# Kernel tuning notes

Hardware: AMD Instinct MI355X
Metric: run time of the kernel (lower is better)

Reference implementation:

```python
import jax, jax.numpy as jnp
import numpy as np

B, T_Q, T_K, H = 16, 1024, 1024, 1024


def _linear_params(key, fan_in, fan_out):
    kw, kb = jax.random.split(key)
    bound = 1.0 / np.sqrt(fan_in)
    W = jax.random.uniform(kw, (fan_out, fan_in), jnp.float32, -bound, bound)
    b = jax.random.uniform(kb, (fan_out,), jnp.float32, -bound, bound)
    return W, b


def setup_inputs() -> dict:
    key = jax.random.key(0)
    ks = jax.random.split(key, 6)
    query = jax.random.normal(ks[0], (B, T_Q, H), jnp.float32)
    keys = jax.random.normal(ks[1], (B, T_K, H), jnp.float32)
    values = jax.random.normal(ks[2], (B, T_K, H), jnp.float32)
    Wq, bq = _linear_params(ks[3], H, H)
    Wk, bk = _linear_params(ks[4], H, H)
    Wo, bo = _linear_params(ks[5], H, H)
    return {"query": query, "keys": keys, "values": values,
            "Wq": Wq, "bq": bq, "Wk": Wk, "bk": bk, "Wo": Wo, "bo": bo}


def reference(query, keys, values, Wq, bq, Wk, bk, Wo, bo):
    # Linear projections (torch Linear: x @ W.T + b)
    q = jnp.einsum('bth,oh->bto', query, Wq) + bq   # (B, T_Q, H)
    k = jnp.einsum('bsh,oh->bso', keys, Wk) + bk    # (B, T_K, H)
    # Unscaled scores -> softmax over key axis (dropout is identity at eval)
    scores = jnp.einsum('bto,bso->bts', q, k)       # (B, T_Q, T_K)
    attn = jax.nn.softmax(scores, axis=-1)
    ctx = jnp.einsum('bts,bsh->bth', attn, values)  # note: raw values, value_fc unused in source
    ctx = ctx / jnp.sqrt(jnp.float32(values.shape[1]))
    out = jnp.einsum('bth,oh->bto', ctx, Wo) + bo
    return out
```

## Files before the change

kernel.cpp:

```cpp
#include <hip/hip_runtime.h>
#include <math.h>

typedef __attribute__((ext_vector_type(4))) float f32x4;
typedef __attribute__((ext_vector_type(8))) _Float16 h16x8;
typedef __attribute__((ext_vector_type(8))) short s16x8;
typedef __attribute__((ext_vector_type(4))) short s16x4;

__device__ inline unsigned short f2h(float f) {
    union { _Float16 h; unsigned short u; } v; v.h = (_Float16)f; return v.u;
}
__device__ inline float h2f(unsigned short u) {
    union { unsigned short u; _Float16 h; } v; v.u = u; return (float)v.h;
}

__device__ inline void async16(const void* g, void* l) {
    __builtin_amdgcn_global_load_lds(
        (const __attribute__((address_space(1))) unsigned int*)g,
        (__attribute__((address_space(3))) unsigned int*)l, 16, 0, 0);
}

__device__ inline void xcd_swizzle(int& bx, int& by, int& bz) {
    const long gx = gridDim.x, gy = gridDim.y;
    const long nwg = gx * gy * (long)gridDim.z;
    const long hw  = ((long)blockIdx.z * gy + blockIdx.y) * gx + blockIdx.x;
    const long qq = nwg >> 3, rr = nwg & 7;
    const long xcd = hw & 7, pos = hw >> 3;
    const long lg = (xcd < rr) ? xcd * (qq + 1) + pos
                               : rr * (qq + 1) + (xcd - rr) * qq + pos;
    bx = (int)(lg % gx);
    const long rem = lg / gx;
    by = (int)(rem % gy);
    bz = (int)(rem / gy);
}

#define BM2 128
#define BN2 256
#define BK2 32

__device__ inline h16x8 ld_frag32(const char* smem, unsigned base, int row, int q) {
    const int lr = row >> 1;
    const int slot = (((row & 1) << 2) | q) ^ (lr & 7);
    return *(const h16x8*)(smem + base + (unsigned)(lr * 128 + slot * 16));
}

template<int OM>
__global__ __launch_bounds__(512, 4)
void gemm128(const unsigned short* __restrict__ A,
             const unsigned short* __restrict__ B,
             const float* __restrict__ bias,
             void* __restrict__ C, int N, int lenK, int pitch,
             long sA, long sB, long sC, long sBias, float scale)
{
    __shared__ __align__(16) char smem[49152];

    const int tid  = threadIdx.x;
    const int wv   = tid >> 6;
    const int lane = tid & 63;
    const int wr = wv >> 2, wc = wv & 3;
    const int lrow = lane & 15;
    const int kq   = lane >> 4;

    int bx, by, bz; xcd_swizzle(bx, by, bz);
    const int n0 = bx * BN2;
    const int m0 = by * BM2;

    const unsigned short* Ag = A + (long)bz * sA;
    const unsigned short* Bg = B + (long)bz * sB;
    const int NT = lenK / BK2;

    auto srcRQ = [](int i, int& r, int& q) {
        int lr = i >> 3;
        int sl = (i & 7) ^ (lr & 7);
        r = (lr << 1) | (sl >> 2);
        q = sl & 3;
    };

    auto stage = [&](int t) {
        const unsigned db = (unsigned)((t & 1) * 24576);
        {
            int r, q; srcRQ(tid, r, q);
            async16((const char*)Ag + ((long)(m0 + r) * pitch + t * BK2 + q * 8) * 2,
                    smem + db + (unsigned)(wv << 10));
        }
#pragma unroll
        for (int l = 0; l < 2; ++l) {
            int r, q; srcRQ(l * 512 + tid, r, q);
            async16((const char*)Bg + ((long)(n0 + r) * pitch + t * BK2 + q * 8) * 2,
                    smem + db + 8192u + (unsigned)(l * 8192) + (unsigned)(wv << 10));
        }
    };

    f32x4 acc[4][4];
#pragma unroll
    for (int i = 0; i < 4; ++i)
#pragma unroll
        for (int j = 0; j < 4; ++j) acc[i][j] = (f32x4){0.f, 0.f, 0.f, 0.f};

    const unsigned Abase = (unsigned)(wr * 4096);
    const unsigned Bbase = 8192u + (unsigned)(wc * 4096);

    stage(0);
    __syncthreads();

#pragma unroll 2
    for (int t = 0; t < NT; ++t) {
        const unsigned db = (unsigned)((t & 1) * 24576);
        if (t + 1 < NT) stage(t + 1);
        h16x8 afr[4], bfr[4];
#pragma unroll
        for (int f = 0; f < 4; ++f) {
            afr[f] = ld_frag32(smem, db + Abase, f * 16 + lrow, kq);
            bfr[f] = ld_frag32(smem, db + Bbase, f * 16 + lrow, kq);
        }
#pragma unroll
        for (int mi = 0; mi < 4; ++mi)
#pragma unroll
            for (int j = 0; j < 4; ++j)
                acc[mi][j] = __builtin_amdgcn_mfma_f32_16x16x32_f16(
                    afr[mi], bfr[j], acc[mi][j], 0, 0, 0);
        __syncthreads();
    }

#pragma unroll
    for (int j = 0; j < 4; ++j) {
        const int col = n0 + wc * 64 + j * 16 + lrow;
        const float bb = bias ? bias[(long)bz * sBias + col] : 0.f;
#pragma unroll
        for (int mi = 0; mi < 4; ++mi) {
#pragma unroll
            for (int r = 0; r < 4; ++r) {
                const long row = m0 + wr * 64 + mi * 16 + (lane >> 4) * 4 + r;
                const float v = acc[mi][j][r] * scale + bb;
                const long idx = (long)bz * sC + row * (long)N + col;
                if constexpr (OM == 0) ((float*)C)[idx] = v;
                else                   ((unsigned short*)C)[idx] = f2h(v);
            }
        }
    }
}


__global__ __launch_bounds__(256)
void conv2_f16(const float* __restrict__ a, const float* __restrict__ b,
               unsigned short* __restrict__ oa, unsigned short* __restrict__ ob)
{
    const long i = ((long)blockIdx.x * 256 + threadIdx.x) * 8;
    const float* in = blockIdx.y ? b : a;
    unsigned short* out = blockIdx.y ? ob : oa;
    f32x4 v0 = __builtin_nontemporal_load((const f32x4*)(in + i));
    f32x4 v1 = __builtin_nontemporal_load((const f32x4*)(in + i + 4));
    s16x8 o = {(short)f2h(v0.x), (short)f2h(v0.y), (short)f2h(v0.z), (short)f2h(v0.w),
               (short)f2h(v1.x), (short)f2h(v1.y), (short)f2h(v1.z), (short)f2h(v1.w)};
    __builtin_nontemporal_store(o, (s16x8*)(out + i));
}

__global__ __launch_bounds__(256)
void conv_f16(const float* __restrict__ in, unsigned short* __restrict__ out, int n)
{
    int i = (blockIdx.x * 256 + threadIdx.x) * 4;
    if (i >= n) return;
    f32x4 v = *(const f32x4*)(in + i);
    s16x4 o = {(short)f2h(v.x), (short)f2h(v.y), (short)f2h(v.z), (short)f2h(v.w)};
    *(s16x4*)(out + i) = o;
}

__global__ __launch_bounds__(256)
void transpose_vals(const float* __restrict__ in, unsigned short* __restrict__ out)
{
    __shared__ float tile[32][33];
    const int h0 = blockIdx.x * 32, t0 = blockIdx.y * 32;
    for (int z = blockIdx.z; z < 16; z += gridDim.z) {
        const long base = (long)z * 1024 * 1024;
        __syncthreads();
        for (int i = threadIdx.y; i < 32; i += 8)
            tile[i][threadIdx.x] = in[base + (long)(t0 + i) * 1024 + h0 + threadIdx.x];
        __syncthreads();
        for (int i = threadIdx.y; i < 32; i += 8)
            out[base + (long)(h0 + i) * 1024 + t0 + threadIdx.x] = f2h(tile[threadIdx.x][i]);
    }
}

__global__ __launch_bounds__(256)
void transpose2_f16(const float* __restrict__ inA, const float* __restrict__ inB,
                    unsigned short* __restrict__ outA, unsigned short* __restrict__ outB)
{
    __shared__ float tile[32][33];
    const float* in = blockIdx.z ? inB : inA;
    unsigned short* out = blockIdx.z ? outB : outA;
    const int h0 = blockIdx.x * 32, t0 = blockIdx.y * 32;
    for (int i = threadIdx.y; i < 32; i += 8)
        tile[i][threadIdx.x] = in[(long)(t0 + i) * 1024 + h0 + threadIdx.x];
    __syncthreads();
    for (int i = threadIdx.y; i < 32; i += 8)
        out[(long)(h0 + i) * 1024 + t0 + threadIdx.x] = f2h(tile[threadIdx.x][i]);
}

__global__ __launch_bounds__(256)
void w2_kernel(const float* __restrict__ Wk, const float* __restrict__ bq,
               float* __restrict__ w2)
{
    __shared__ float part[4][64];
    const int tx = threadIdx.x & 63;
    const int ty = threadIdx.x >> 6;
    const int h  = blockIdx.x * 64 + tx;
    float s = 0.f;
    for (int o = ty * 256; o < ty * 256 + 256; ++o)
        s = fmaf(Wk[(long)o * 1024 + h], bq[o], s);
    part[ty][tx] = s;
    __syncthreads();
    if (ty == 0) w2[h] = part[0][tx] + part[1][tx] + part[2][tx] + part[3][tx];
}

__global__ __launch_bounds__(256)
void matvec_v(const unsigned short* __restrict__ Xk, const float* __restrict__ w2,
              float* __restrict__ v)
{
    const int wave = threadIdx.x >> 6, lane = threadIdx.x & 63;
    const long row = (long)blockIdx.x * 4 + wave;
    const unsigned short* p = Xk + row * 1024 + lane * 16;
    float s = 0.f;
#pragma unroll
    for (int c = 0; c < 2; ++c) {
        s16x8 hv = *(const s16x8*)(p + c * 8);
#pragma unroll
        for (int e = 0; e < 8; ++e)
            s = fmaf(h2f((unsigned short)hv[e]), w2[lane * 16 + c * 8 + e], s);
    }
#pragma unroll
    for (int off = 1; off < 64; off <<= 1) s += __shfl_xor(s, off);
    if (lane == 0) v[row] = s;
}

__global__ __launch_bounds__(256)
void reduce4(const float* __restrict__ p, unsigned short* __restrict__ MT)
{
    const long i = ((long)blockIdx.x * 256 + threadIdx.x) * 4;
    const long S = 1024L * 1024;
    f32x4 a = *(const f32x4*)(p + i);
    f32x4 b = *(const f32x4*)(p + S + i);
    f32x4 c = *(const f32x4*)(p + 2 * S + i);
    f32x4 d = *(const f32x4*)(p + 3 * S + i);
    s16x4 o = {(short)f2h(a.x + b.x + c.x + d.x), (short)f2h(a.y + b.y + c.y + d.y),
               (short)f2h(a.z + b.z + c.z + d.z), (short)f2h(a.w + b.w + c.w + d.w)};
    *(s16x4*)(MT + i) = o;
}

__global__ __launch_bounds__(256)
void softmax_wave(unsigned short* __restrict__ S)
{
    const int wave = threadIdx.x >> 6, lane = threadIdx.x & 63;
    for (long row = (long)blockIdx.x * 4 + wave; row < 16384; row += (long)gridDim.x * 4) {
        unsigned short* p = S + row * 1024;
        s16x8 ra = *(s16x8*)(p + lane * 8);
        s16x8 rb = *(s16x8*)(p + 512 + lane * 8);
        float va[8], vb[8];
        float m = -3.0e38f;
#pragma unroll
        for (int e = 0; e < 8; ++e) {
            va[e] = h2f((unsigned short)ra[e]); m = fmaxf(m, va[e]);
            vb[e] = h2f((unsigned short)rb[e]); m = fmaxf(m, vb[e]);
        }
#pragma unroll
        for (int off = 1; off < 64; off <<= 1) m = fmaxf(m, __shfl_xor(m, off));
        float s = 0.f;
#pragma unroll
        for (int e = 0; e < 8; ++e) {
            va[e] = expf(va[e] - m); s += va[e];
            vb[e] = expf(vb[e] - m); s += vb[e];
        }
#pragma unroll
        for (int off = 1; off < 64; off <<= 1) s += __shfl_xor(s, off);
        const float inv = 1.f / s;
        s16x8 oa, ob;
#pragma unroll
        for (int e = 0; e < 8; ++e) {
            oa[e] = (short)f2h(va[e] * inv);
            ob[e] = (short)f2h(vb[e] * inv);
        }
        *(s16x8*)(p + lane * 8)       = oa;
        *(s16x8*)(p + 512 + lane * 8) = ob;
    }
}

extern "C" void kernel_launch(void* const* d_in, const int* in_sizes, int n_in,
                              void* d_out, int out_size, void* d_ws, size_t ws_size,
                              hipStream_t stream)
{
    const float* query  = (const float*)d_in[0];
    const float* keys   = (const float*)d_in[1];
    const float* values = (const float*)d_in[2];
    const float* Wq     = (const float*)d_in[3];
    const float* bq     = (const float*)d_in[4];
    const float* Wk     = (const float*)d_in[5];
    const float* bk     = (const float*)d_in[6];
    const float* Wo     = (const float*)d_in[7];
    const float* bo     = (const float*)d_in[8];
    (void)bk;

    const int  T = 1024, H = 1024;
    const long NE = 16384L * 1024;
    const long NW = 1024L * 1024;

    size_t need = (size_t)(NE * 4 + NW * 12 + 40960) * sizeof(unsigned short);
    if (ws_size < need) return;

    unsigned short* ws   = (unsigned short*)d_ws;
    unsigned short* Xq   = ws;
    unsigned short* Xk   = Xq + NE;
    unsigned short* vT   = Xk + NE;
    unsigned short* P1   = vT + NE;
    unsigned short* WqT  = P1 + NE;
    unsigned short* WkT  = WqT + NW;
    unsigned short* Woh  = WkT + NW;
    unsigned short* MT   = Woh + NW;
    float*          part = (float*)(MT + NW);
    float*          w2   = (float*)(MT + NW * 9);
    float*          vvec = w2 + 1024;
    unsigned short* sc   = Xq;
    unsigned short* ctx  = P1;

    conv2_f16<<<dim3(8192, 2, 1), 256, 0, stream>>>(query, keys, Xq, Xk);
    transpose2_f16<<<dim3(32, 32, 2), dim3(32, 8), 0, stream>>>(Wq, Wk, WqT, WkT);
    conv_f16<<<1024, 256, 0, stream>>>(Wo, Woh, (int)NW);
    transpose_vals<<<dim3(32, 32, 4), dim3(32, 8), 0, stream>>>(values, vT);
    w2_kernel<<<16, 256, 0, stream>>>(Wk, bq, w2);

    gemm128<0><<<dim3(4, 8, 4), 512, 0, stream>>>(
        WkT, WqT, nullptr, part, 1024, 256, 1024, 256, 256, (long)NW, 0, 1.f);
    reduce4<<<1024, 256, 0, stream>>>(part, MT);

    gemm128<1><<<dim3(4, 128, 1), 512, 0, stream>>>(
        Xq, MT, nullptr, P1, H, H, H, 0, 0, 0, 0, 1.f);

    matvec_v<<<4096, 256, 0, stream>>>(Xk, w2, vvec);

    gemm128<1><<<dim3(4, 8, 16), 512, 0, stream>>>(
        P1, Xk, vvec, sc, T, H, H,
        (long)T * H, (long)T * H, (long)T * T, (long)T, 1.f);

    softmax_wave<<<2048, 256, 0, stream>>>(sc);

    gemm128<1><<<dim3(4, 8, 16), 512, 0, stream>>>(
        sc, vT, nullptr, ctx, H, T, T,
        (long)T * T, (long)T * H, (long)T * H, 0, 1.f / 32.f);

    gemm128<0><<<dim3(4, 128, 1), 512, 0, stream>>>(
        ctx, Woh, bo, d_out, H, H, H, 0, 0, 0, 0, 1.f);
}
```

Before: 285.7 us.

## Switch GEMMs to 256x256 tiles with 4 waves and fuse key matvec into conversion

New measurement: 293.6 us. 2.8% more time.

```diff
diff --git a/kernel.cpp b/kernel.cpp
--- a/kernel.cpp
+++ b/kernel.cpp
@@ -33,8 +33,6 @@
     bz = (int)(rem / gy);
 }
 
-#define BM2 128
-#define BN2 256
 #define BK2 32
 
 __device__ inline h16x8 ld_frag32(const char* smem, unsigned base, int row, int q) {
@@ -44,25 +42,25 @@
 }
 
 template<int OM>
-__global__ __launch_bounds__(512, 4)
-void gemm128(const unsigned short* __restrict__ A,
-             const unsigned short* __restrict__ B,
-             const float* __restrict__ bias,
-             void* __restrict__ C, int N, int lenK, int pitch,
-             long sA, long sB, long sC, long sBias, float scale)
-{
-    __shared__ __align__(16) char smem[49152];
+__global__ __launch_bounds__(256, 1)
+void gemm256w4(const unsigned short* __restrict__ A,
+               const unsigned short* __restrict__ B,
+               const float* __restrict__ bias,
+               void* __restrict__ C, int N, int lenK, int pitch,
+               long sA, long sB, long sC, long sBias, float scale)
+{
+    __shared__ __align__(16) char smem[65536];
 
     const int tid  = threadIdx.x;
     const int wv   = tid >> 6;
     const int lane = tid & 63;
-    const int wr = wv >> 2, wc = wv & 3;
+    const int wr = wv >> 1, wc = wv & 1;
     const int lrow = lane & 15;
     const int kq   = lane >> 4;
 
     int bx, by, bz; xcd_swizzle(bx, by, bz);
-    const int n0 = bx * BN2;
-    const int m0 = by * BM2;
+    const int n0 = bx * 256;
+    const int m0 = by * 256;
 
     const unsigned short* Ag = A + (long)bz * sA;
     const unsigned short* Bg = B + (long)bz * sB;
@@ -76,60 +74,58 @@
     };
 
     auto stage = [&](int t) {
-        const unsigned db = (unsigned)((t & 1) * 24576);
-        {
-            int r, q; srcRQ(tid, r, q);
+        const unsigned db = (unsigned)((t & 1) * 32768);
+#pragma unroll
+        for (int l = 0; l < 4; ++l) {
+            int r, q; srcRQ(l * 256 + tid, r, q);
             async16((const char*)Ag + ((long)(m0 + r) * pitch + t * BK2 + q * 8) * 2,
-                    smem + db + (unsigned)(wv << 10));
-        }
-#pragma unroll
-        for (int l = 0; l < 2; ++l) {
-            int r, q; srcRQ(l * 512 + tid, r, q);
+                    smem + db + (unsigned)(l * 4096) + (unsigned)(wv << 10));
+        }
+#pragma unroll
+        for (int l = 0; l < 4; ++l) {
+            int r, q; srcRQ(l * 256 + tid, r, q);
             async16((const char*)Bg + ((long)(n0 + r) * pitch + t * BK2 + q * 8) * 2,
-                    smem + db + 8192u + (unsigned)(l * 8192) + (unsigned)(wv << 10));
+                    smem + db + 16384u + (unsigned)(l * 4096) + (unsigned)(wv << 10));
         }
     };
 
-    f32x4 acc[4][4];
-#pragma unroll
-    for (int i = 0; i < 4; ++i)
-#pragma unroll
-        for (int j = 0; j < 4; ++j) acc[i][j] = (f32x4){0.f, 0.f, 0.f, 0.f};
-
-    const unsigned Abase = (unsigned)(wr * 4096);
-    const unsigned Bbase = 8192u + (unsigned)(wc * 4096);
+    f32x4 acc[8][8];
+#pragma unroll
+    for (int i = 0; i < 8; ++i)
+#pragma unroll
+        for (int j = 0; j < 8; ++j) acc[i][j] = (f32x4){0.f, 0.f, 0.f, 0.f};
 
     stage(0);
     __syncthreads();
 
 #pragma unroll 2
     for (int t = 0; t < NT; ++t) {
-        const unsigned db = (unsigned)((t & 1) * 24576);
+        const unsigned db = (unsigned)((t & 1) * 32768);
         if (t + 1 < NT) stage(t + 1);
-        h16x8 afr[4], bfr[4];
-#pragma unroll
-        for (int f = 0; f < 4; ++f) {
-            afr[f] = ld_frag32(smem, db + Abase, f * 16 + lrow, kq);
-            bfr[f] = ld_frag32(smem, db + Bbase, f * 16 + lrow, kq);
-        }
-#pragma unroll
-        for (int mi = 0; mi < 4; ++mi)
-#pragma unroll
-            for (int j = 0; j < 4; ++j)
+        h16x8 afr[8], bfr[8];
+#pragma unroll
+        for (int f = 0; f < 8; ++f) {
+            afr[f] = ld_frag32(smem, db,          wr * 128 + f * 16 + lrow, kq);
+            bfr[f] = ld_frag32(smem, db + 16384u, wc * 128 + f * 16 + lrow, kq);
+        }
+#pragma unroll
+        for (int mi = 0; mi < 8; ++mi)
+#pragma unroll
+            for (int j = 0; j < 8; ++j)
                 acc[mi][j] = __builtin_amdgcn_mfma_f32_16x16x32_f16(
                     afr[mi], bfr[j], acc[mi][j], 0, 0, 0);
         __syncthreads();
     }
 
 #pragma unroll
-    for (int j = 0; j < 4; ++j) {
-        const int col = n0 + wc * 64 + j * 16 + lrow;
+    for (int j = 0; j < 8; ++j) {
+        const int col = n0 + wc * 128 + j * 16 + lrow;
         const float bb = bias ? bias[(long)bz * sBias + col] : 0.f;
 #pragma unroll
-        for (int mi = 0; mi < 4; ++mi) {
+        for (int mi = 0; mi < 8; ++mi) {
 #pragma unroll
             for (int r = 0; r < 4; ++r) {
-                const long row = m0 + wr * 64 + mi * 16 + (lane >> 4) * 4 + r;
+                const long row = m0 + wr * 128 + mi * 16 + (lane >> 4) * 4 + r;
                 const float v = acc[mi][j][r] * scale + bb;
                 const long idx = (long)bz * sC + row * (long)N + col;
                 if constexpr (OM == 0) ((float*)C)[idx] = v;
@@ -142,7 +138,8 @@
 
 __global__ __launch_bounds__(256)
 void conv2_f16(const float* __restrict__ a, const float* __restrict__ b,
-               unsigned short* __restrict__ oa, unsigned short* __restrict__ ob)
+               unsigned short* __restrict__ oa, unsigned short* __restrict__ ob,
+               const float* __restrict__ w2, float* __restrict__ vvec)
 {
     const long i = ((long)blockIdx.x * 256 + threadIdx.x) * 8;
     const float* in = blockIdx.y ? b : a;
@@ -152,6 +149,23 @@
     s16x8 o = {(short)f2h(v0.x), (short)f2h(v0.y), (short)f2h(v0.z), (short)f2h(v0.w),
                (short)f2h(v1.x), (short)f2h(v1.y), (short)f2h(v1.z), (short)f2h(v1.w)};
     __builtin_nontemporal_store(o, (s16x8*)(out + i));
+
+    if (blockIdx.y) {
+        const int col = (threadIdx.x & 127) * 8;
+        f32x4 w0 = *(const f32x4*)(w2 + col);
+        f32x4 w1 = *(const f32x4*)(w2 + col + 4);
+        float s = v0.x * w0.x + v0.y * w0.y + v0.z * w0.z + v0.w * w0.w
+                + v1.x * w1.x + v1.y * w1.y + v1.z * w1.z + v1.w * w1.w;
+#pragma unroll
+        for (int off = 1; off < 64; off <<= 1) s += __shfl_xor(s, off);
+        __shared__ float red[4];
+        const int wave = threadIdx.x >> 6, lane = threadIdx.x & 63;
+        if (lane == 0) red[wave] = s;
+        __syncthreads();
+        if (threadIdx.x < 2)
+            vvec[(long)blockIdx.x * 2 + threadIdx.x] =
+                red[threadIdx.x * 2] + red[threadIdx.x * 2 + 1];
+    }
 }
 
 __global__ __launch_bounds__(256)
@@ -209,26 +223,6 @@
     part[ty][tx] = s;
     __syncthreads();
     if (ty == 0) w2[h] = part[0][tx] + part[1][tx] + part[2][tx] + part[3][tx];
-}
-
-__global__ __launch_bounds__(256)
-void matvec_v(const unsigned short* __restrict__ Xk, const float* __restrict__ w2,
-              float* __restrict__ v)
-{
-    const int wave = threadIdx.x >> 6, lane = threadIdx.x & 63;
-    const long row = (long)blockIdx.x * 4 + wave;
-    const unsigned short* p = Xk + row * 1024 + lane * 16;
-    float s = 0.f;
-#pragma unroll
-    for (int c = 0; c < 2; ++c) {
-        s16x8 hv = *(const s16x8*)(p + c * 8);
-#pragma unroll
-        for (int e = 0; e < 8; ++e)
-            s = fmaf(h2f((unsigned short)hv[e]), w2[lane * 16 + c * 8 + e], s);
-    }
-#pragma unroll
-    for (int off = 1; off < 64; off <<= 1) s += __shfl_xor(s, off);
-    if (lane == 0) v[row] = s;
 }
 
 __global__ __launch_bounds__(256)
@@ -319,31 +313,29 @@
     unsigned short* sc   = Xq;
     unsigned short* ctx  = P1;
 
-    conv2_f16<<<dim3(8192, 2, 1), 256, 0, stream>>>(query, keys, Xq, Xk);
+    w2_kernel<<<16, 256, 0, stream>>>(Wk, bq, w2);
+    conv2_f16<<<dim3(8192, 2, 1), 256, 0, stream>>>(query, keys, Xq, Xk, w2, vvec);
     transpose2_f16<<<dim3(32, 32, 2), dim3(32, 8), 0, stream>>>(Wq, Wk, WqT, WkT);
     conv_f16<<<1024, 256, 0, stream>>>(Wo, Woh, (int)NW);
     transpose_vals<<<dim3(32, 32, 4), dim3(32, 8), 0, stream>>>(values, vT);
-    w2_kernel<<<16, 256, 0, stream>>>(Wk, bq, w2);
-
-    gemm128<0><<<dim3(4, 8, 4), 512, 0, stream>>>(
+
+    gemm256w4<0><<<dim3(4, 4, 4), 256, 0, stream>>>(
         WkT, WqT, nullptr, part, 1024, 256, 1024, 256, 256, (long)NW, 0, 1.f);
     reduce4<<<1024, 256, 0, stream>>>(part, MT);
 
-    gemm128<1><<<dim3(4, 128, 1), 512, 0, stream>>>(
+    gemm256w4<1><<<dim3(4, 64, 1), 256, 0, stream>>>(
         Xq, MT, nullptr, P1, H, H, H, 0, 0, 0, 0, 1.f);
 
-    matvec_v<<<4096, 256, 0, stream>>>(Xk, w2, vvec);
-
-    gemm128<1><<<dim3(4, 8, 16), 512, 0, stream>>>(
+    gemm256w4<1><<<dim3(4, 4, 16), 256, 0, stream>>>(
         P1, Xk, vvec, sc, T, H, H,
         (long)T * H, (long)T * H, (long)T * T, (long)T, 1.f);
 
     softmax_wave<<<2048, 256, 0, stream>>>(sc);
 
-    gemm128<1><<<dim3(4, 8, 16), 512, 0, stream>>>(
+    gemm256w4<1><<<dim3(4, 4, 16), 256, 0, stream>>>(
         sc, vT, nullptr, ctx, H, T, T,
         (long)T * T, (long)T * H, (long)T * H, 0, 1.f / 32.f);
 
-    gemm128<0><<<dim3(4, 128, 1), 512, 0, stream>>>(
+    gemm256w4<0><<<dim3(4, 64, 1), 256, 0, stream>>>(
         ctx, Woh, bo, d_out, H, H, H, 0, 0, 0, 0, 1.f);
 }
```
